# Performance work log

Hardware: AMD Instinct MI355X
Metric: run time of the kernel (lower is better)

The kernel has to match this reference:

```python
import jax, jax.numpy as jnp
import numpy as np

KAPPA = 0.1          # temperature for sinkhorn routing
SINK_ITERS = 3
SINK_EPS = 1e-6
NORM_EPS = 1e-12     # F.normalize clamp
LOG_EPS = 2.220446049250313e-16  # np.finfo(float).eps
K_TOP = 1


def _l2norm(v, axis=-1):
    n = jnp.sqrt(jnp.sum(v * v, axis=axis, keepdims=True))
    return v / jnp.maximum(n, NORM_EPS)


def _sinkhorn(log_alpha):
    # log_alpha: [K, N]
    L = jnp.exp(log_alpha)
    for _ in range(SINK_ITERS):
        L = L / (jnp.sum(L, axis=1, keepdims=True) + SINK_EPS)
        L = L / (jnp.sum(L, axis=0, keepdims=True) + SINK_EPS)
    return L


def setup_inputs() -> dict:
    key = jax.random.key(0)
    ks = jax.random.split(key, 16)
    dim = 1024
    N = 32768
    lora_dim = [8, 16, 32, 48, 64, 96, 128]
    inp = {
        "x": jax.random.normal(ks[0], (N, dim), dtype=jnp.float32),
        "prototypes": jax.random.normal(ks[1], (7, dim), dtype=jnp.float32),
    }
    for e, d in enumerate(lora_dim):
        # torch Linear weight: [out_features, in_features]
        inp[f"A{e}"] = jax.random.normal(ks[2 + 2 * e], (d, dim), dtype=jnp.float32) * (1.0 / np.sqrt(dim))
        inp[f"B{e}"] = jax.random.normal(ks[3 + 2 * e], (dim, d), dtype=jnp.float32) * (1.0 / np.sqrt(d))
    return inp


def reference(x, prototypes, A0, B0, A1, B1, A2, B2, A3, B3, A4, B4, A5, B5, A6, B6):
    A = [A0, A1, A2, A3, A4, A5, A6]
    B = [B0, B1, B2, B3, B4, B5, B6]
    N = x.shape[0]
    num_experts = len(A)

    # --- sinkhorn routing: gates [N, K] ---
    x_n = _l2norm(x)                       # [N, D]
    p_n = _l2norm(prototypes)              # [K, D]
    sim = jnp.einsum('kd,nd->kn', p_n, x_n)  # [K, N]
    L = _sinkhorn(sim / KAPPA)             # [K, N] doubly-stochastic-ish
    gates_full = L.T                       # [N, K]

    # --- top-k sparsification (k=1) ---
    top_vals, top_idx = jax.lax.top_k(gates_full, K_TOP)  # [N, k]
    gates = jnp.zeros_like(gates_full).at[jnp.arange(N)[:, None], top_idx].set(top_vals)

    # --- per-expert LoRA + weighted log-space combine ---
    # combine: out[b] = log( sum_e gates[b,e] * exp(B_e(A_e(x_b))) ), eps floor
    combined = jnp.zeros_like(x)
    for e in range(num_experts):
        y = jnp.einsum('nr,dr->nd', jnp.einsum('nd,rd->nr', x, A[e]), B[e])  # [N, D]
        combined = combined + gates[:, e:e + 1] * jnp.exp(y)
    combined = jnp.where(combined == 0, LOG_EPS, combined)
    return jnp.log(combined)
```

## Files before the change

### kernel.cpp

```cpp
#include <hip/hip_runtime.h>
#include <math.h>

#define NTOK 32768
#define DIM  1024
#define NE   7

#define PN_OFF   0
#define R1_OFF   7168
#define R2_OFF   7176
#define R3_OFF   7184
#define CNT_OFF  7192
#define PR1_OFF  7200
#define PR2_OFF  23584
#define PR3_OFF  24608
#define E0_OFF   25632
#define LG_OFF   287776
#define LIST_OFF 320544
#define A16_OFF  549920
#define B16_OFF  754720

#define SEPS 1e-6f

typedef __attribute__((ext_vector_type(8))) short short8v;
typedef __attribute__((ext_vector_type(4))) float f32x4;

constexpr int DV[7]   = {8, 16, 32, 48, 64, 96, 128};
constexpr int DPV[7]  = {32, 32, 32, 64, 64, 96, 128};
constexpr int DAPV[7] = {16, 16, 32, 48, 64, 96, 128};
constexpr int AOV[7]  = {0, 16384, 32768, 65536, 114688, 180224, 278528};
constexpr int BOV[7]  = {0, 32768, 65536, 98304, 163840, 229376, 327680};

struct ExpPtrs { const float* A[NE]; const float* B[NE]; };

__device__ __forceinline__ short f2bf(float f) {
  union { float f; unsigned u; } v; v.f = f;
  return (short)((v.u + 0x7FFFu + ((v.u >> 16) & 1u)) >> 16);
}

__device__ __forceinline__ float wsum(float v) {
  #pragma unroll
  for (int off = 32; off > 0; off >>= 1) v += __shfl_xor(v, off);
  return v;
}

__device__ __forceinline__ float dot4acc(float4 a, float4 b, float acc) {
  acc = fmaf(a.x, b.x, acc);
  acc = fmaf(a.y, b.y, acc);
  acc = fmaf(a.z, b.z, acc);
  acc = fmaf(a.w, b.w, acc);
  return acc;
}

__device__ __forceinline__ void ecfg(int e, int& d, int& dp, int& dap, int& ao, int& bo) {
  switch (e) {
    case 0: d = 8;   dp = 32;  dap = 16;  ao = 0;      bo = 0;      break;
    case 1: d = 16;  dp = 32;  dap = 16;  ao = 16384;  bo = 32768;  break;
    case 2: d = 32;  dp = 32;  dap = 32;  ao = 32768;  bo = 65536;  break;
    case 3: d = 48;  dp = 64;  dap = 48;  ao = 65536;  bo = 98304;  break;
    case 4: d = 64;  dp = 64;  dap = 64;  ao = 114688; bo = 163840; break;
    case 5: d = 96;  dp = 96;  dap = 96;  ao = 180224; bo = 229376; break;
    default: d = 128; dp = 128; dap = 128; ao = 278528; bo = 327680; break;
  }
}

__global__ __launch_bounds__(256) void k_conv(ExpPtrs p, short* __restrict__ A16,
                                              short* __restrict__ B16,
                                              const float* __restrict__ proto,
                                              float* __restrict__ wsf,
                                              int* __restrict__ counts) {
  const int e = blockIdx.y;
  const int tid = threadIdx.x;
  int d, dp, dap, ao, bo;
  ecfg(e, d, dp, dap, ao, bo);

  if (blockIdx.x == 0) {
    __shared__ float pred[4];
    if (e == 0 && tid < 8) counts[tid] = 0;
    const int w = tid >> 6, lane = tid & 63;
    float v4[4], ss = 0.f;
    #pragma unroll
    for (int i = 0; i < 4; ++i) {
      v4[i] = proto[e * DIM + tid + 256 * i];
      ss = fmaf(v4[i], v4[i], ss);
    }
    ss = wsum(ss);
    if (lane == 0) pred[w] = ss;
    __syncthreads();
    float tot = ((pred[0] + pred[1]) + pred[2]) + pred[3];
    float inv = 1.f / fmaxf(sqrtf(tot), 1e-12f);
    #pragma unroll
    for (int i = 0; i < 4; ++i)
      wsf[PN_OFF + e * DIM + tid + 256 * i] = v4[i] * inv;
  }

  const float* A = p.A[e];
  const float* B = p.B[e];
  short* Ad = A16 + ao;
  short* Bd = B16 + bo;
  const int t0 = blockIdx.x * 256 + tid;
  for (int i = t0; i < dap * DIM; i += 16 * 256) {
    int row = i >> 10;
    Ad[i] = (row < d) ? f2bf(A[i]) : (short)0;
  }
  for (int i = t0; i < DIM * dp; i += 16 * 256) {
    int j = i / dp, r = i - j * dp;
    Bd[i] = (r < d) ? f2bf(B[j * d + r]) : (short)0;
  }
}

__global__ __launch_bounds__(256) void k_sim(const float* __restrict__ x,
                                             const float* __restrict__ wsf,
                                             float* __restrict__ e0,
                                             float* __restrict__ pr1) {
  const int tid = threadIdx.x, w = tid >> 6, lane = tid & 63;
  const float4* pn4 = (const float4*)(wsf + PN_OFF);
  const int gw = blockIdx.x * 4 + w;
  float r1a[NE] = {0.f, 0.f, 0.f, 0.f, 0.f, 0.f, 0.f};
  for (int it = 0; it < 4; ++it) {
    const int n = gw + 8192 * it;
    const float4* xr4 = (const float4*)(x + (size_t)n * DIM);
    float xx = 0.f;
    float dk[NE] = {0.f, 0.f, 0.f, 0.f, 0.f, 0.f, 0.f};
    #pragma unroll
    for (int i = 0; i < 4; ++i) {
      float4 xv = xr4[lane + 64 * i];
      xx = dot4acc(xv, xv, xx);
      #pragma unroll
      for (int k = 0; k < NE; ++k)
        dk[k] = dot4acc(xv, pn4[k * 256 + lane + 64 * i], dk[k]);
    }
    xx = wsum(xx);
    #pragma unroll
    for (int k = 0; k < NE; ++k) dk[k] = wsum(dk[k]);
    if (lane == 0) {
      float nrm = fmaxf(sqrtf(xx), 1e-12f);
      #pragma unroll
      for (int k = 0; k < NE; ++k) {
        float ev = expf((dk[k] / nrm) / 0.1f);
        e0[(size_t)n * 8 + k] = ev;
        r1a[k] += ev;
      }
    }
  }
  __shared__ float red[4][8];
  if (lane == 0) {
    #pragma unroll
    for (int k = 0; k < NE; ++k) red[w][k] = r1a[k];
  }
  __syncthreads();
  if (tid == 0) {
    #pragma unroll
    for (int k = 0; k < NE; ++k)
      pr1[blockIdx.x * 8 + k] = ((red[0][k] + red[1][k]) + red[2][k]) + red[3][k];
  }
}

#define SUM7(l) (((((((l)[0] + (l)[1]) + (l)[2]) + (l)[3]) + (l)[4]) + (l)[5]) + (l)[6])

template<int DEPTH>
__global__ __launch_bounds__(256) void k_pass(const float* __restrict__ e0,
                                              float* __restrict__ wsf,
                                              const float* __restrict__ src, int nb,
                                              float* __restrict__ prOut,
                                              int* __restrict__ counts,
                                              int* __restrict__ list,
                                              float* __restrict__ lgv) {
  __shared__ float red2[8][33];
  __shared__ float Rcur[8];
  const int tid = threadIdx.x;
  {
    const int k = tid & 7, m = tid >> 3;
    float a = 0.f;
    for (int b = m; b < nb; b += 32) a += src[b * 8 + k];
    red2[k][m] = a;
    __syncthreads();
    if (tid < 8) {
      float s = 0.f;
      for (int mm = 0; mm < 32; ++mm) s += red2[tid][mm];
      Rcur[tid] = s;
      if (blockIdx.x == 0) {
        int roff = (DEPTH == 1) ? R1_OFF : (DEPTH == 2) ? R2_OFF : R3_OFF;
        wsf[roff + tid] = s;
      }
    }
    __syncthreads();
  }

  const int n = blockIdx.x * 256 + tid;
  float4 v0 = *(const float4*)(e0 + (size_t)n * 8);
  float4 v1 = *(const float4*)(e0 + (size_t)n * 8 + 4);
  float l[NE] = {v0.x, v0.y, v0.z, v0.w, v1.x, v1.y, v1.z};
  {
    const float* R1 = (DEPTH == 1) ? Rcur : (wsf + R1_OFF);
    #pragma unroll
    for (int k = 0; k < NE; ++k) l[k] = l[k] / (R1[k] + SEPS);
    float C = SUM7(l);
    #pragma unroll
    for (int k = 0; k < NE; ++k) l[k] = l[k] / (C + SEPS);
  }
  if constexpr (DEPTH >= 2) {
    const float* R2 = (DEPTH == 2) ? Rcur : (wsf + R2_OFF);
    #pragma unroll
    for (int k = 0; k < NE; ++k) l[k] = l[k] / (R2[k] + SEPS);
    float C = SUM7(l);
    #pragma unroll
    for (int k = 0; k < NE; ++k) l[k] = l[k] / (C + SEPS);
  }
  if constexpr (DEPTH >= 3) {
    const float* R3 = Rcur;
    #pragma unroll
    for (int k = 0; k < NE; ++k) l[k] = l[k] / (R3[k] + SEPS);
    float C = SUM7(l);
    #pragma unroll
    for (int k = 0; k < NE; ++k) l[k] = l[k] / (C + SEPS);
  }
  if constexpr (DEPTH == 3) {
    float best = l[0]; int be = 0;
    #pragma unroll
    for (int k = 1; k < NE; ++k) {
      if (l[k] > best) { best = l[k]; be = k; }
    }
    __shared__ int lcnt[8];
    __shared__ int wbase[4][8];
    __shared__ int gbase[8];
    const int w = tid >> 6, lane = tid & 63;
    if (tid < 8) lcnt[tid] = 0;
    __syncthreads();
    int rank = 0;
    #pragma unroll
    for (int k = 0; k < NE; ++k) {
      unsigned long long m = __ballot(be == k);
      if (lane == 0) wbase[w][k] = m ? atomicAdd(&lcnt[k], (int)__popcll(m)) : 0;
      if (be == k) rank = (int)__popcll(m & ((1ull << lane) - 1ull));
    }
    __syncthreads();
    if (tid < 8) gbase[tid] = lcnt[tid] ? atomicAdd(&counts[tid], lcnt[tid]) : 0;
    __syncthreads();
    int pos = gbase[be] + wbase[w][be] + rank;
    list[be * NTOK + pos] = n;
    lgv[n] = logf(best);
  } else {
    __shared__ float red[NE][256];
    #pragma unroll
    for (int k = 0; k < NE; ++k) red[k][tid] = l[k];
    __syncthreads();
    for (int off = 128; off > 0; off >>= 1) {
      if (tid < off) {
        #pragma unroll
        for (int k = 0; k < NE; ++k) red[k][tid] += red[k][tid + off];
      }
      __syncthreads();
    }
    if (tid < NE) prOut[blockIdx.x * 8 + tid] = red[tid][0];
  }
}

template<int E>
__device__ void expert_mfma(const float* __restrict__ x,
                            const short* __restrict__ A16,
                            const short* __restrict__ B16,
                            const int* __restrict__ list_e,
                            const float* __restrict__ lg,
                            int cnt, float* __restrict__ out,
                            char* lds) {
  constexpr int DP = DPV[E], DAP = DAPV[E];
  constexpr int NT1 = DAP / 16;
  constexpr int KS2 = DP / 32;
  constexpr int PP  = DAP + 4;
  constexpr int SP  = DP + 8;
  float* P = (float*)lds;
  short* T = (short*)(lds + 2 * 16 * PP * 4);

  const short* Am = A16 + AOV[E];
  const short* Bp = B16 + BOV[E];
  const int tid = threadIdx.x;
  const int w = tid >> 6, lane = tid & 63;
  const int lo = lane & 15, hi = lane >> 4;
  const int m0 = blockIdx.x * 16;

  const int myTok = list_e[min(m0 + lo, cnt - 1)];
  const float* xp = x + (size_t)myTok * DIM + w * 256 + hi * 8;
  const short* ApL = Am + lo * DIM + w * 256 + hi * 8;

  f32x4 acc1[NT1];
  #pragma unroll
  for (int t = 0; t < NT1; ++t) acc1[t] = (f32x4){0.f, 0.f, 0.f, 0.f};

  float4 nx0 = *(const float4*)(xp);
  float4 nx1 = *(const float4*)(xp + 4);
  #pragma unroll
  for (int kc = 0; kc < 256; kc += 32) {
    float4 x0 = nx0, x1 = nx1;
    if (kc + 32 < 256) {
      nx0 = *(const float4*)(xp + kc + 32);
      nx1 = *(const float4*)(xp + kc + 36);
    }
    short8v af;
    af[0] = f2bf(x0.x); af[1] = f2bf(x0.y); af[2] = f2bf(x0.z); af[3] = f2bf(x0.w);
    af[4] = f2bf(x1.x); af[5] = f2bf(x1.y); af[6] = f2bf(x1.z); af[7] = f2bf(x1.w);
    #pragma unroll
    for (int t = 0; t < NT1; ++t) {
      short8v bf = *(const short8v*)(ApL + t * 16 * DIM + kc);
      acc1[t] = __builtin_amdgcn_mfma_f32_16x16x32_bf16(af, bf, acc1[t], 0, 0, 0);
    }
  }

  float* Pw = P + (w & 1) * 16 * PP;
  if (w < 2) {
    #pragma unroll
    for (int t = 0; t < NT1; ++t)
      #pragma unroll
      for (int j = 0; j < 4; ++j)
        Pw[(hi * 4 + j) * PP + t * 16 + lo] = acc1[t][j];
  }
  __syncthreads();
  if (w >= 2) {
    #pragma unroll
    for (int t = 0; t < NT1; ++t)
      #pragma unroll
      for (int j = 0; j < 4; ++j)
        Pw[(hi * 4 + j) * PP + t * 16 + lo] += acc1[t][j];
  }
  __syncthreads();
  for (int i = tid; i < 16 * DP; i += 256) {
    int r = i / DP, c = i - r * DP;
    float v = (c < DAP) ? (P[r * PP + c] + P[(16 + r) * PP + c]) : 0.f;
    T[r * SP + c] = f2bf(v);
  }
  __syncthreads();

  short8v tf[KS2];
  #pragma unroll
  for (int ks = 0; ks < KS2; ++ks)
    tf[ks] = *(const short8v*)(T + lo * SP + ks * 32 + hi * 8);

  float  lgvr[4];
  float* op[4];
  #pragma unroll
  for (int j = 0; j < 4; ++j) {
    int t = list_e[min(m0 + hi * 4 + j, cnt - 1)];
    lgvr[j] = lg[t];
    op[j] = out + (size_t)t * DIM + w * 256 + lo;
  }

  const short* BpL = Bp + (size_t)(w * 256 + lo) * DP + hi * 8;
  #pragma unroll 4
  for (int nt = 0; nt < 16; ++nt) {
    f32x4 acc = (f32x4){0.f, 0.f, 0.f, 0.f};
    #pragma unroll
    for (int ks = 0; ks < KS2; ++ks) {
      short8v bf = *(const short8v*)(BpL + (size_t)nt * 16 * DP + ks * 32);
      acc = __builtin_amdgcn_mfma_f32_16x16x32_bf16(tf[ks], bf, acc, 0, 0, 0);
    }
    #pragma unroll
    for (int j = 0; j < 4; ++j)
      op[j][nt * 16] = acc[j] + lgvr[j];
  }
}

__global__ __launch_bounds__(256) void k_expert(const float* __restrict__ x,
                                                const short* __restrict__ A16,
                                                const short* __restrict__ B16,
                                                const int* __restrict__ list,
                                                const float* __restrict__ lg,
                                                const int* __restrict__ counts,
                                                float* __restrict__ out) {
  __shared__ __align__(16) char lds[21248];
  const int e = blockIdx.y;
  const int cnt = counts[e];
  if ((int)blockIdx.x * 16 >= cnt) return;
  switch (e) {
    case 0: expert_mfma<0>(x, A16, B16, list + 0 * NTOK, lg, cnt, out, lds); break;
    case 1: expert_mfma<1>(x, A16, B16, list + 1 * NTOK, lg, cnt, out, lds); break;
    case 2: expert_mfma<2>(x, A16, B16, list + 2 * NTOK, lg, cnt, out, lds); break;
    case 3: expert_mfma<3>(x, A16, B16, list + 3 * NTOK, lg, cnt, out, lds); break;
    case 4: expert_mfma<4>(x, A16, B16, list + 4 * NTOK, lg, cnt, out, lds); break;
    case 5: expert_mfma<5>(x, A16, B16, list + 5 * NTOK, lg, cnt, out, lds); break;
    case 6: expert_mfma<6>(x, A16, B16, list + 6 * NTOK, lg, cnt, out, lds); break;
  }
}

extern "C" void kernel_launch(void* const* d_in, const int* in_sizes, int n_in,
                              void* d_out, int out_size, void* d_ws, size_t ws_size,
                              hipStream_t stream) {
  const float* x     = (const float*)d_in[0];
  const float* proto = (const float*)d_in[1];
  ExpPtrs p;
  for (int e = 0; e < NE; ++e) {
    p.A[e] = (const float*)d_in[2 + 2 * e];
    p.B[e] = (const float*)d_in[3 + 2 * e];
  }
  float* wsf = (float*)d_ws;
  int*   wsi = (int*)d_ws;
  short* A16 = (short*)(wsf + A16_OFF);
  short* B16 = (short*)(wsf + B16_OFF);
  float* out = (float*)d_out;

  k_conv<<<dim3(16, NE), 256, 0, stream>>>(p, A16, B16, proto, wsf, wsi + CNT_OFF);
  k_sim<<<2048, 256, 0, stream>>>(x, wsf, wsf + E0_OFF, wsf + PR1_OFF);
  k_pass<1><<<128, 256, 0, stream>>>(wsf + E0_OFF, wsf, wsf + PR1_OFF, 2048,
                                     wsf + PR2_OFF, nullptr, nullptr, nullptr);
  k_pass<2><<<128, 256, 0, stream>>>(wsf + E0_OFF, wsf, wsf + PR2_OFF, 128,
                                     wsf + PR3_OFF, nullptr, nullptr, nullptr);
  k_pass<3><<<128, 256, 0, stream>>>(wsf + E0_OFF, wsf, wsf + PR3_OFF, 128,
                                     nullptr, wsi + CNT_OFF, wsi + LIST_OFF, wsf + LG_OFF);
  k_expert<<<dim3(2048, NE), 256, 0, stream>>>(x, A16, B16, wsi + LIST_OFF,
                                               wsf + LG_OFF, wsi + CNT_OFF, out);
}
```

Baseline: 195.0 us.

## Flatten expert grid into compact tile list and alias LDS staging buffers

Replaces the 2048x7 expert grid, where most blocks exit early, with a 1D grid of 2055 blocks. Each block walks the per-expert counts to find its expert and tile, so almost no launched blocks are idle. The bf16 staging buffer T now aliases the fp32 partial-sum buffer P: values are read into registers, a barrier is taken, then written back. This shrinks LDS per block so more blocks can be resident, at the cost of an extra barrier and a short serial scan over counts in every block.

```diff
diff --git a/kernel.cpp b/kernel.cpp
--- a/kernel.cpp
+++ b/kernel.cpp
@@ -261,7 +261,7 @@
                             const short* __restrict__ B16,
                             const int* __restrict__ list_e,
                             const float* __restrict__ lg,
-                            int cnt, float* __restrict__ out,
+                            int cnt, int tile, float* __restrict__ out,
                             char* lds) {
   constexpr int DP = DPV[E], DAP = DAPV[E];
   constexpr int NT1 = DAP / 16;
@@ -269,14 +269,14 @@
   constexpr int PP  = DAP + 4;
   constexpr int SP  = DP + 8;
   float* P = (float*)lds;
-  short* T = (short*)(lds + 2 * 16 * PP * 4);
+  short* T = (short*)lds;
 
   const short* Am = A16 + AOV[E];
   const short* Bp = B16 + BOV[E];
   const int tid = threadIdx.x;
   const int w = tid >> 6, lane = tid & 63;
   const int lo = lane & 15, hi = lane >> 4;
-  const int m0 = blockIdx.x * 16;
+  const int m0 = tile * 16;
 
   const int myTok = list_e[min(m0 + lo, cnt - 1)];
   const float* xp = x + (size_t)myTok * DIM + w * 256 + hi * 8;
@@ -322,10 +322,26 @@
         Pw[(hi * 4 + j) * PP + t * 16 + lo] += acc1[t][j];
   }
   __syncthreads();
-  for (int i = tid; i < 16 * DP; i += 256) {
-    int r = i / DP, c = i - r * DP;
-    float v = (c < DAP) ? (P[r * PP + c] + P[(16 + r) * PP + c]) : 0.f;
-    T[r * SP + c] = f2bf(v);
+  constexpr int NITEM = (16 * DP + 255) / 256;
+  float vloc[NITEM];
+  #pragma unroll
+  for (int it = 0; it < NITEM; ++it) {
+    int i = tid + it * 256;
+    float v = 0.f;
+    if (i < 16 * DP) {
+      int r = i / DP, c = i - r * DP;
+      if (c < DAP) v = P[r * PP + c] + P[(16 + r) * PP + c];
+    }
+    vloc[it] = v;
+  }
+  __syncthreads();
+  #pragma unroll
+  for (int it = 0; it < NITEM; ++it) {
+    int i = tid + it * 256;
+    if (i < 16 * DP) {
+      int r = i / DP, c = i - r * DP;
+      T[r * SP + c] = f2bf(vloc[it]);
+    }
   }
   __syncthreads();
 
@@ -365,18 +381,24 @@
                                                 const float* __restrict__ lg,
                                                 const int* __restrict__ counts,
                                                 float* __restrict__ out) {
-  __shared__ __align__(16) char lds[21248];
-  const int e = blockIdx.y;
-  const int cnt = counts[e];
-  if ((int)blockIdx.x * 16 >= cnt) return;
+  __shared__ __align__(16) char lds[16896];
+  int rem = blockIdx.x;
+  int e = 0, cnt;
+  while (true) {
+    cnt = counts[e];
+    int tiles = (cnt + 15) >> 4;
+    if (rem < tiles) break;
+    rem -= tiles;
+    if (++e == NE) return;
+  }
   switch (e) {
-    case 0: expert_mfma<0>(x, A16, B16, list + 0 * NTOK, lg, cnt, out, lds); break;
-    case 1: expert_mfma<1>(x, A16, B16, list + 1 * NTOK, lg, cnt, out, lds); break;
-    case 2: expert_mfma<2>(x, A16, B16, list + 2 * NTOK, lg, cnt, out, lds); break;
-    case 3: expert_mfma<3>(x, A16, B16, list + 3 * NTOK, lg, cnt, out, lds); break;
-    case 4: expert_mfma<4>(x, A16, B16, list + 4 * NTOK, lg, cnt, out, lds); break;
-    case 5: expert_mfma<5>(x, A16, B16, list + 5 * NTOK, lg, cnt, out, lds); break;
-    case 6: expert_mfma<6>(x, A16, B16, list + 6 * NTOK, lg, cnt, out, lds); break;
+    case 0: expert_mfma<0>(x, A16, B16, list + 0 * NTOK, lg, cnt, rem, out, lds); break;
+    case 1: expert_mfma<1>(x, A16, B16, list + 1 * NTOK, lg, cnt, rem, out, lds); break;
+    case 2: expert_mfma<2>(x, A16, B16, list + 2 * NTOK, lg, cnt, rem, out, lds); break;
+    case 3: expert_mfma<3>(x, A16, B16, list + 3 * NTOK, lg, cnt, rem, out, lds); break;
+    case 4: expert_mfma<4>(x, A16, B16, list + 4 * NTOK, lg, cnt, rem, out, lds); break;
+    case 5: expert_mfma<5>(x, A16, B16, list + 5 * NTOK, lg, cnt, rem, out, lds); break;
+    case 6: expert_mfma<6>(x, A16, B16, list + 6 * NTOK, lg, cnt, rem, out, lds); break;
   }
 }
 
@@ -404,6 +426,6 @@
                                      wsf + PR3_OFF, nullptr, nullptr, nullptr);
   k_pass<3><<<128, 256, 0, stream>>>(wsf + E0_OFF, wsf, wsf + PR3_OFF, 128,
                                      nullptr, wsi + CNT_OFF, wsi + LIST_OFF, wsf + LG_OFF);
-  k_expert<<<dim3(2048, NE), 256, 0, stream>>>(x, A16, B16, wsi + LIST_OFF,
-                                               wsf + LG_OFF, wsi + CNT_OFF, out);
-}
+  k_expert<<<2055, 256, 0, stream>>>(x, A16, B16, wsi + LIST_OFF,
+                                     wsf + LG_OFF, wsi + CNT_OFF, out);
+}
```

Result: no change. 192.9 us (-1.1%).

## Fuse all-expert A projection into similarity pass and compact expert launch

Applied to the files above, without the earlier changes.

The similarity kernel now streams each x tile once and, besides the prototype dot products, computes the A projections for all seven experts with MFMA, writing a bf16 low-rank buffer per token. The expert kernel then reads only this small buffer instead of re-reading x rows through the routing list, which removes the per-expert A GEMM and the LDS reduction. A flat 1D grid walks the expert counts so only populated tiles are launched. The cost is computing A projections for all experts on every token (about seven times the A work) plus an extra workspace write and read.

```diff
diff --git a/kernel.cpp b/kernel.cpp
--- a/kernel.cpp
+++ b/kernel.cpp
@@ -4,6 +4,7 @@
 #define NTOK 32768
 #define DIM  1024
 #define NE   7
+#define TROW 448
 
 #define PN_OFF   0
 #define R1_OFF   7168
@@ -18,6 +19,8 @@
 #define LIST_OFF 320544
 #define A16_OFF  549920
 #define B16_OFF  754720
+#define TALL_OFF_BYTES 3936384
+#define NBLK 2055
 
 #define SEPS 1e-6f
 
@@ -29,6 +32,10 @@
 constexpr int DAPV[7] = {16, 16, 32, 48, 64, 96, 128};
 constexpr int AOV[7]  = {0, 16384, 32768, 65536, 114688, 180224, 278528};
 constexpr int BOV[7]  = {0, 32768, 65536, 98304, 163840, 229376, 327680};
+constexpr int APRE[7] = {0, 32, 64, 96, 160, 224, 320};
+constexpr int TCOL[25] = {0, 32, 64, 80, 96, 112, 128, 160, 176, 192, 208,
+                          224, 240, 256, 272, 288, 304,
+                          320, 336, 352, 368, 384, 400, 416, 432};
 
 struct ExpPtrs { const float* A[NE]; const float* B[NE]; };
 
@@ -108,50 +115,106 @@
   }
 }
 
-__global__ __launch_bounds__(256) void k_sim(const float* __restrict__ x,
-                                             const float* __restrict__ wsf,
-                                             float* __restrict__ e0,
-                                             float* __restrict__ pr1) {
-  const int tid = threadIdx.x, w = tid >> 6, lane = tid & 63;
-  const float4* pn4 = (const float4*)(wsf + PN_OFF);
-  const int gw = blockIdx.x * 4 + w;
-  float r1a[NE] = {0.f, 0.f, 0.f, 0.f, 0.f, 0.f, 0.f};
-  for (int it = 0; it < 4; ++it) {
-    const int n = gw + 8192 * it;
-    const float4* xr4 = (const float4*)(x + (size_t)n * DIM);
-    float xx = 0.f;
-    float dk[NE] = {0.f, 0.f, 0.f, 0.f, 0.f, 0.f, 0.f};
-    #pragma unroll
-    for (int i = 0; i < 4; ++i) {
-      float4 xv = xr4[lane + 64 * i];
-      xx = dot4acc(xv, xv, xx);
+__global__ __launch_bounds__(512, 4) void k_simT(const float* __restrict__ x,
+                                                 const short* __restrict__ A16,
+                                                 const float* __restrict__ wsf,
+                                                 float* __restrict__ e0,
+                                                 float* __restrict__ pr1,
+                                                 short* __restrict__ Tall) {
+  __shared__ __align__(16) short As[400 * 40];
+  __shared__ float pnS[7][32];
+  __shared__ float prS[4][16][8];
+  const int tid = threadIdx.x;
+  const int n0 = blockIdx.x * 64;
+
+  for (int i = tid; i < 64 * 48; i += 512) {
+    int r = i / 48, c = i - r * 48;
+    int col = (c < 16) ? (16 + c) : ((c < 32) ? (32 + c) : (112 + c));
+    Tall[(size_t)(n0 + r) * TROW + col] = 0;
+  }
+
+  const int w = tid >> 6, lane = tid & 63, lo = lane & 15, hi = lane >> 4;
+  const int mh = w >> 1, nh = w & 1;
+  const int tokBase = n0 + mh * 16;
+  const int ts = nh * 12;
+  const float* xp = x + (size_t)(tokBase + lo) * DIM + hi * 8;
+  const float* PN = wsf + PN_OFF;
+
+  f32x4 acc[13];
+  #pragma unroll
+  for (int t = 0; t < 13; ++t) acc[t] = (f32x4){0.f, 0.f, 0.f, 0.f};
+  float dk[7] = {0.f, 0.f, 0.f, 0.f, 0.f, 0.f, 0.f};
+  float xx = 0.f;
+
+  for (int kc = 0; kc < DIM; kc += 32) {
+    for (int i = tid; i < 1600; i += 512) {
+      int r = i >> 2, q = i & 3;
+      *(short8v*)&As[r * 40 + q * 8] =
+          *(const short8v*)(A16 + (size_t)r * DIM + kc + q * 8);
+    }
+    if (tid < 224) pnS[tid >> 5][tid & 31] = PN[(tid >> 5) * DIM + kc + (tid & 31)];
+    __syncthreads();
+
+    float4 x0 = *(const float4*)(xp + kc);
+    float4 x1 = *(const float4*)(xp + kc + 4);
+    short8v af;
+    af[0] = f2bf(x0.x); af[1] = f2bf(x0.y); af[2] = f2bf(x0.z); af[3] = f2bf(x0.w);
+    af[4] = f2bf(x1.x); af[5] = f2bf(x1.y); af[6] = f2bf(x1.z); af[7] = f2bf(x1.w);
+
+    if (nh == 0) {
+      xx = dot4acc(x0, x0, dot4acc(x1, x1, xx));
       #pragma unroll
-      for (int k = 0; k < NE; ++k)
-        dk[k] = dot4acc(xv, pn4[k * 256 + lane + 64 * i], dk[k]);
-    }
-    xx = wsum(xx);
-    #pragma unroll
-    for (int k = 0; k < NE; ++k) dk[k] = wsum(dk[k]);
-    if (lane == 0) {
+      for (int k = 0; k < 7; ++k) {
+        float4 p0 = *(const float4*)&pnS[k][hi * 8];
+        float4 p1 = *(const float4*)&pnS[k][hi * 8 + 4];
+        dk[k] = dot4acc(x0, p0, dot4acc(x1, p1, dk[k]));
+      }
+    }
+    #pragma unroll
+    for (int tt = 0; tt < 13; ++tt) {
+      short8v bf = *(const short8v*)&As[(16 * (ts + tt) + lo) * 40 + hi * 8];
+      acc[tt] = __builtin_amdgcn_mfma_f32_16x16x32_bf16(af, bf, acc[tt], 0, 0, 0);
+    }
+    __syncthreads();
+  }
+
+  const int tw = 12 + nh;
+  #pragma unroll
+  for (int tt = 0; tt < 13; ++tt) {
+    if (tt < tw) {
+      int col = TCOL[ts + tt] + lo;
+      #pragma unroll
+      for (int j = 0; j < 4; ++j)
+        Tall[(size_t)(tokBase + hi * 4 + j) * TROW + col] = f2bf(acc[tt][j]);
+    }
+  }
+
+  if (nh == 0) {
+    #pragma unroll
+    for (int k = 0; k < 7; ++k) {
+      dk[k] += __shfl_xor(dk[k], 16);
+      dk[k] += __shfl_xor(dk[k], 32);
+    }
+    xx += __shfl_xor(xx, 16);
+    xx += __shfl_xor(xx, 32);
+    if (hi == 0) {
       float nrm = fmaxf(sqrtf(xx), 1e-12f);
+      int n = tokBase + lo;
       #pragma unroll
-      for (int k = 0; k < NE; ++k) {
+      for (int k = 0; k < 7; ++k) {
         float ev = expf((dk[k] / nrm) / 0.1f);
         e0[(size_t)n * 8 + k] = ev;
-        r1a[k] += ev;
+        prS[mh][lo][k] = ev;
       }
-    }
-  }
-  __shared__ float red[4][8];
-  if (lane == 0) {
-    #pragma unroll
-    for (int k = 0; k < NE; ++k) red[w][k] = r1a[k];
+      prS[mh][lo][7] = 0.f;
+    }
   }
   __syncthreads();
-  if (tid == 0) {
-    #pragma unroll
-    for (int k = 0; k < NE; ++k)
-      pr1[blockIdx.x * 8 + k] = ((red[0][k] + red[1][k]) + red[2][k]) + red[3][k];
+  if (tid < 8) {
+    float s = 0.f;
+    for (int m2 = 0; m2 < 4; ++m2)
+      for (int l2 = 0; l2 < 16; ++l2) s += prS[m2][l2][tid];
+    pr1[blockIdx.x * 8 + tid] = s;
   }
 }
 
@@ -255,96 +318,46 @@
   }
 }
 
+__device__ __forceinline__ bool walk(int bid, const int* counts,
+                                     int& e, int& tile, int& cnt) {
+  int rem = bid; e = 0;
+  while (true) {
+    cnt = counts[e];
+    int tiles = (cnt + 15) >> 4;
+    if (rem < tiles) { tile = rem; return true; }
+    rem -= tiles;
+    if (++e == NE) return false;
+  }
+}
+
 template<int E>
-__device__ void expert_mfma(const float* __restrict__ x,
-                            const short* __restrict__ A16,
-                            const short* __restrict__ B16,
-                            const int* __restrict__ list_e,
-                            const float* __restrict__ lg,
-                            int cnt, float* __restrict__ out,
-                            char* lds) {
-  constexpr int DP = DPV[E], DAP = DAPV[E];
-  constexpr int NT1 = DAP / 16;
+__device__ void phB_impl(const short* __restrict__ Bp,
+                         const short* __restrict__ Tall,
+                         const int* __restrict__ list_e,
+                         const float* __restrict__ lg,
+                         int cnt, int tile, float* __restrict__ out) {
+  constexpr int DP = DPV[E];
   constexpr int KS2 = DP / 32;
-  constexpr int PP  = DAP + 4;
-  constexpr int SP  = DP + 8;
-  float* P = (float*)lds;
-  short* T = (short*)(lds + 2 * 16 * PP * 4);
-
-  const short* Am = A16 + AOV[E];
-  const short* Bp = B16 + BOV[E];
   const int tid = threadIdx.x;
   const int w = tid >> 6, lane = tid & 63;
   const int lo = lane & 15, hi = lane >> 4;
-  const int m0 = blockIdx.x * 16;
+  const int m0 = tile * 16;
 
   const int myTok = list_e[min(m0 + lo, cnt - 1)];
-  const float* xp = x + (size_t)myTok * DIM + w * 256 + hi * 8;
-  const short* ApL = Am + lo * DIM + w * 256 + hi * 8;
-
-  f32x4 acc1[NT1];
-  #pragma unroll
-  for (int t = 0; t < NT1; ++t) acc1[t] = (f32x4){0.f, 0.f, 0.f, 0.f};
-
-  float4 nx0 = *(const float4*)(xp);
-  float4 nx1 = *(const float4*)(xp + 4);
-  #pragma unroll
-  for (int kc = 0; kc < 256; kc += 32) {
-    float4 x0 = nx0, x1 = nx1;
-    if (kc + 32 < 256) {
-      nx0 = *(const float4*)(xp + kc + 32);
-      nx1 = *(const float4*)(xp + kc + 36);
-    }
-    short8v af;
-    af[0] = f2bf(x0.x); af[1] = f2bf(x0.y); af[2] = f2bf(x0.z); af[3] = f2bf(x0.w);
-    af[4] = f2bf(x1.x); af[5] = f2bf(x1.y); af[6] = f2bf(x1.z); af[7] = f2bf(x1.w);
-    #pragma unroll
-    for (int t = 0; t < NT1; ++t) {
-      short8v bf = *(const short8v*)(ApL + t * 16 * DIM + kc);
-      acc1[t] = __builtin_amdgcn_mfma_f32_16x16x32_bf16(af, bf, acc1[t], 0, 0, 0);
-    }
-  }
-
-  float* Pw = P + (w & 1) * 16 * PP;
-  if (w < 2) {
-    #pragma unroll
-    for (int t = 0; t < NT1; ++t)
-      #pragma unroll
-      for (int j = 0; j < 4; ++j)
-        Pw[(hi * 4 + j) * PP + t * 16 + lo] = acc1[t][j];
-  }
-  __syncthreads();
-  if (w >= 2) {
-    #pragma unroll
-    for (int t = 0; t < NT1; ++t)
-      #pragma unroll
-      for (int j = 0; j < 4; ++j)
-        Pw[(hi * 4 + j) * PP + t * 16 + lo] += acc1[t][j];
-  }
-  __syncthreads();
-  for (int i = tid; i < 16 * DP; i += 256) {
-    int r = i / DP, c = i - r * DP;
-    float v = (c < DAP) ? (P[r * PP + c] + P[(16 + r) * PP + c]) : 0.f;
-    T[r * SP + c] = f2bf(v);
-  }
-  __syncthreads();
-
   short8v tf[KS2];
   #pragma unroll
   for (int ks = 0; ks < KS2; ++ks)
-    tf[ks] = *(const short8v*)(T + lo * SP + ks * 32 + hi * 8);
-
-  float  lgvr[4];
-  float* op[4];
+    tf[ks] = *(const short8v*)(Tall + (size_t)myTok * TROW + APRE[E] + ks * 32 + hi * 8);
+
+  int tok[4]; float lgvr[4];
   #pragma unroll
   for (int j = 0; j < 4; ++j) {
-    int t = list_e[min(m0 + hi * 4 + j, cnt - 1)];
-    lgvr[j] = lg[t];
-    op[j] = out + (size_t)t * DIM + w * 256 + lo;
+    tok[j] = list_e[min(m0 + hi * 4 + j, cnt - 1)];
+    lgvr[j] = lg[tok[j]];
   }
 
   const short* BpL = Bp + (size_t)(w * 256 + lo) * DP + hi * 8;
-  #pragma unroll 4
+  #pragma unroll 1
   for (int nt = 0; nt < 16; ++nt) {
     f32x4 acc = (f32x4){0.f, 0.f, 0.f, 0.f};
     #pragma unroll
@@ -354,29 +367,27 @@
     }
     #pragma unroll
     for (int j = 0; j < 4; ++j)
-      op[j][nt * 16] = acc[j] + lgvr[j];
-  }
-}
-
-__global__ __launch_bounds__(256) void k_expert(const float* __restrict__ x,
-                                                const short* __restrict__ A16,
-                                                const short* __restrict__ B16,
+      out[(size_t)tok[j] * DIM + w * 256 + nt * 16 + lo] = acc[j] + lgvr[j];
+  }
+}
+
+__global__ __launch_bounds__(256, 8) void k_phB(const short* __restrict__ B16,
+                                                const short* __restrict__ Tall,
                                                 const int* __restrict__ list,
                                                 const float* __restrict__ lg,
                                                 const int* __restrict__ counts,
                                                 float* __restrict__ out) {
-  __shared__ __align__(16) char lds[21248];
-  const int e = blockIdx.y;
-  const int cnt = counts[e];
-  if ((int)blockIdx.x * 16 >= cnt) return;
+  int bid = ((int)blockIdx.x * 1024) % NBLK;
+  int e, tile, cnt;
+  if (!walk(bid, counts, e, tile, cnt)) return;
   switch (e) {
-    case 0: expert_mfma<0>(x, A16, B16, list + 0 * NTOK, lg, cnt, out, lds); break;
-    case 1: expert_mfma<1>(x, A16, B16, list + 1 * NTOK, lg, cnt, out, lds); break;
-    case 2: expert_mfma<2>(x, A16, B16, list + 2 * NTOK, lg, cnt, out, lds); break;
-    case 3: expert_mfma<3>(x, A16, B16, list + 3 * NTOK, lg, cnt, out, lds); break;
-    case 4: expert_mfma<4>(x, A16, B16, list + 4 * NTOK, lg, cnt, out, lds); break;
-    case 5: expert_mfma<5>(x, A16, B16, list + 5 * NTOK, lg, cnt, out, lds); break;
-    case 6: expert_mfma<6>(x, A16, B16, list + 6 * NTOK, lg, cnt, out, lds); break;
+    case 0: phB_impl<0>(B16 + BOV[0], Tall, list + 0 * NTOK, lg, cnt, tile, out); break;
+    case 1: phB_impl<1>(B16 + BOV[1], Tall, list + 1 * NTOK, lg, cnt, tile, out); break;
+    case 2: phB_impl<2>(B16 + BOV[2], Tall, list + 2 * NTOK, lg, cnt, tile, out); break;
+    case 3: phB_impl<3>(B16 + BOV[3], Tall, list + 3 * NTOK, lg, cnt, tile, out); break;
+    case 4: phB_impl<4>(B16 + BOV[4], Tall, list + 4 * NTOK, lg, cnt, tile, out); break;
+    case 5: phB_impl<5>(B16 + BOV[5], Tall, list + 5 * NTOK, lg, cnt, tile, out); break;
+    default: phB_impl<6>(B16 + BOV[6], Tall, list + 6 * NTOK, lg, cnt, tile, out); break;
   }
 }
 
@@ -394,16 +405,17 @@
   int*   wsi = (int*)d_ws;
   short* A16 = (short*)(wsf + A16_OFF);
   short* B16 = (short*)(wsf + B16_OFF);
+  short* Tall = (short*)((char*)d_ws + TALL_OFF_BYTES);
   float* out = (float*)d_out;
 
   k_conv<<<dim3(16, NE), 256, 0, stream>>>(p, A16, B16, proto, wsf, wsi + CNT_OFF);
-  k_sim<<<2048, 256, 0, stream>>>(x, wsf, wsf + E0_OFF, wsf + PR1_OFF);
-  k_pass<1><<<128, 256, 0, stream>>>(wsf + E0_OFF, wsf, wsf + PR1_OFF, 2048,
+  k_simT<<<512, 512, 0, stream>>>(x, A16, wsf, wsf + E0_OFF, wsf + PR1_OFF, Tall);
+  k_pass<1><<<128, 256, 0, stream>>>(wsf + E0_OFF, wsf, wsf + PR1_OFF, 512,
                                      wsf + PR2_OFF, nullptr, nullptr, nullptr);
   k_pass<2><<<128, 256, 0, stream>>>(wsf + E0_OFF, wsf, wsf + PR2_OFF, 128,
                                      wsf + PR3_OFF, nullptr, nullptr, nullptr);
   k_pass<3><<<128, 256, 0, stream>>>(wsf + E0_OFF, wsf, wsf + PR3_OFF, 128,
                                      nullptr, wsi + CNT_OFF, wsi + LIST_OFF, wsf + LG_OFF);
-  k_expert<<<dim3(2048, NE), 256, 0, stream>>>(x, A16, B16, wsi + LIST_OFF,
-                                               wsf + LG_OFF, wsi + CNT_OFF, out);
-}
+  k_phB<<<NBLK, 256, 0, stream>>>(B16, Tall, wsi + LIST_OFF, wsf + LG_OFF,
+                                  wsi + CNT_OFF, out);
+}
```

After: 211.0 us. 1.08x slower.

## Re-layout A weights, drop cross-wave K-split reduction, compact expert tile grid

Applied to the files above, without the earlier changes.

Stores the bf16 A weights in a chunked image laid out by 32-column K-chunks, so each wave computes the full K=1024 projection for its 16-token tile on its own. This removes the LDS partial-sum reduction and the three block-wide barriers. The 2D grid of 2048x7 blocks, most of which exited early, becomes a compact 1D grid of 2055 tiles mapped onto experts by a prefix walk over counts, with a strided permutation of block ids. Each wave now redundantly reads all of x and A for the tile, so every block does four times the first-GEMM work in exchange for no synchronisation, and occupancy is set to 4 blocks via launch bounds.

```diff
diff --git a/kernel.cpp b/kernel.cpp
--- a/kernel.cpp
+++ b/kernel.cpp
@@ -16,8 +16,9 @@
 #define E0_OFF   25632
 #define LG_OFF   287776
 #define LIST_OFF 320544
-#define A16_OFF  549920
 #define B16_OFF  754720
+#define AIMG_OFF_BYTES 3936384
+#define NBLK 2055
 
 #define SEPS 1e-6f
 
@@ -27,14 +28,18 @@
 constexpr int DV[7]   = {8, 16, 32, 48, 64, 96, 128};
 constexpr int DPV[7]  = {32, 32, 32, 64, 64, 96, 128};
 constexpr int DAPV[7] = {16, 16, 32, 48, 64, 96, 128};
-constexpr int AOV[7]  = {0, 16384, 32768, 65536, 114688, 180224, 278528};
 constexpr int BOV[7]  = {0, 32768, 65536, 98304, 163840, 229376, 327680};
+constexpr int RSV[7]  = {0, 16, 32, 64, 112, 176, 272};
 
 struct ExpPtrs { const float* A[NE]; const float* B[NE]; };
 
 __device__ __forceinline__ short f2bf(float f) {
   union { float f; unsigned u; } v; v.f = f;
   return (short)((v.u + 0x7FFFu + ((v.u >> 16) & 1u)) >> 16);
+}
+
+__device__ __forceinline__ unsigned packbf(float a, float b) {
+  return (unsigned)(unsigned short)f2bf(a) | ((unsigned)(unsigned short)f2bf(b) << 16);
 }
 
 __device__ __forceinline__ float wsum(float v) {
@@ -51,27 +56,14 @@
   return acc;
 }
 
-__device__ __forceinline__ void ecfg(int e, int& d, int& dp, int& dap, int& ao, int& bo) {
-  switch (e) {
-    case 0: d = 8;   dp = 32;  dap = 16;  ao = 0;      bo = 0;      break;
-    case 1: d = 16;  dp = 32;  dap = 16;  ao = 16384;  bo = 32768;  break;
-    case 2: d = 32;  dp = 32;  dap = 32;  ao = 32768;  bo = 65536;  break;
-    case 3: d = 48;  dp = 64;  dap = 48;  ao = 65536;  bo = 98304;  break;
-    case 4: d = 64;  dp = 64;  dap = 64;  ao = 114688; bo = 163840; break;
-    case 5: d = 96;  dp = 96;  dap = 96;  ao = 180224; bo = 229376; break;
-    default: d = 128; dp = 128; dap = 128; ao = 278528; bo = 327680; break;
-  }
-}
-
-__global__ __launch_bounds__(256) void k_conv(ExpPtrs p, short* __restrict__ A16,
+__global__ __launch_bounds__(256) void k_conv(ExpPtrs p, short* __restrict__ AIMG,
                                               short* __restrict__ B16,
                                               const float* __restrict__ proto,
                                               float* __restrict__ wsf,
                                               int* __restrict__ counts) {
   const int e = blockIdx.y;
   const int tid = threadIdx.x;
-  int d, dp, dap, ao, bo;
-  ecfg(e, d, dp, dap, ao, bo);
+  const int d = DV[e], dp = DPV[e], dap = DAPV[e], bo = BOV[e], rs = RSV[e];
 
   if (blockIdx.x == 0) {
     __shared__ float pred[4];
@@ -95,16 +87,25 @@
 
   const float* A = p.A[e];
   const float* B = p.B[e];
-  short* Ad = A16 + ao;
+  const int t0 = blockIdx.x * 256 + tid;
+
+  const int tot = dap * 128;
+  for (int i = t0; i < tot; i += 16 * 256) {
+    int lr = i >> 7, rem = i & 127;
+    int c = rem >> 2, q = rem & 3;
+    short8v v = (short8v){0, 0, 0, 0, 0, 0, 0, 0};
+    if (lr < d) {
+      const float* src = A + (size_t)lr * DIM + c * 32 + q * 8;
+      #pragma unroll
+      for (int j = 0; j < 8; ++j) v[j] = f2bf(src[j]);
+    }
+    *(short8v*)&AIMG[c * 12800 + (rs + lr) * 32 + q * 8] = v;
+  }
+
   short* Bd = B16 + bo;
-  const int t0 = blockIdx.x * 256 + tid;
-  for (int i = t0; i < dap * DIM; i += 16 * 256) {
-    int row = i >> 10;
-    Ad[i] = (row < d) ? f2bf(A[i]) : (short)0;
-  }
   for (int i = t0; i < DIM * dp; i += 16 * 256) {
     int j = i / dp, r = i - j * dp;
-    Bd[i] = (r < d) ? f2bf(B[j * d + r]) : (short)0;
+    Bd[i] = (r < d) ? f2bf(B[(size_t)j * d + r]) : (short)0;
   }
 }
 
@@ -257,30 +258,27 @@
 
 template<int E>
 __device__ void expert_mfma(const float* __restrict__ x,
-                            const short* __restrict__ A16,
+                            const short* __restrict__ AIMG,
                             const short* __restrict__ B16,
                             const int* __restrict__ list_e,
                             const float* __restrict__ lg,
-                            int cnt, float* __restrict__ out,
-                            char* lds) {
+                            int cnt, int tile, float* __restrict__ out,
+                            short* Tlds) {
   constexpr int DP = DPV[E], DAP = DAPV[E];
   constexpr int NT1 = DAP / 16;
   constexpr int KS2 = DP / 32;
-  constexpr int PP  = DAP + 4;
   constexpr int SP  = DP + 8;
-  float* P = (float*)lds;
-  short* T = (short*)(lds + 2 * 16 * PP * 4);
-
-  const short* Am = A16 + AOV[E];
+  const int rs = RSV[E];
   const short* Bp = B16 + BOV[E];
   const int tid = threadIdx.x;
   const int w = tid >> 6, lane = tid & 63;
   const int lo = lane & 15, hi = lane >> 4;
-  const int m0 = blockIdx.x * 16;
+  const int m0 = tile * 16;
+  short* T = Tlds + w * 16 * 136;
 
   const int myTok = list_e[min(m0 + lo, cnt - 1)];
-  const float* xp = x + (size_t)myTok * DIM + w * 256 + hi * 8;
-  const short* ApL = Am + lo * DIM + w * 256 + hi * 8;
+  const float* xp = x + (size_t)myTok * DIM + hi * 8;
+  const short* Ab = AIMG + (rs + lo) * 32 + hi * 8;
 
   f32x4 acc1[NT1];
   #pragma unroll
@@ -288,63 +286,49 @@
 
   float4 nx0 = *(const float4*)(xp);
   float4 nx1 = *(const float4*)(xp + 4);
-  #pragma unroll
-  for (int kc = 0; kc < 256; kc += 32) {
+  for (int c = 0; c < 32; ++c) {
     float4 x0 = nx0, x1 = nx1;
-    if (kc + 32 < 256) {
-      nx0 = *(const float4*)(xp + kc + 32);
-      nx1 = *(const float4*)(xp + kc + 36);
+    if (c < 31) {
+      nx0 = *(const float4*)(xp + (c + 1) * 32);
+      nx1 = *(const float4*)(xp + (c + 1) * 32 + 4);
     }
     short8v af;
     af[0] = f2bf(x0.x); af[1] = f2bf(x0.y); af[2] = f2bf(x0.z); af[3] = f2bf(x0.w);
     af[4] = f2bf(x1.x); af[5] = f2bf(x1.y); af[6] = f2bf(x1.z); af[7] = f2bf(x1.w);
+    const short* Ac = Ab + c * 12800;
     #pragma unroll
     for (int t = 0; t < NT1; ++t) {
-      short8v bf = *(const short8v*)(ApL + t * 16 * DIM + kc);
-      acc1[t] = __builtin_amdgcn_mfma_f32_16x16x32_bf16(af, bf, acc1[t], 0, 0, 0);
-    }
-  }
-
-  float* Pw = P + (w & 1) * 16 * PP;
-  if (w < 2) {
-    #pragma unroll
-    for (int t = 0; t < NT1; ++t)
-      #pragma unroll
-      for (int j = 0; j < 4; ++j)
-        Pw[(hi * 4 + j) * PP + t * 16 + lo] = acc1[t][j];
-  }
-  __syncthreads();
-  if (w >= 2) {
-    #pragma unroll
-    for (int t = 0; t < NT1; ++t)
-      #pragma unroll
-      for (int j = 0; j < 4; ++j)
-        Pw[(hi * 4 + j) * PP + t * 16 + lo] += acc1[t][j];
-  }
-  __syncthreads();
-  for (int i = tid; i < 16 * DP; i += 256) {
-    int r = i / DP, c = i - r * DP;
-    float v = (c < DAP) ? (P[r * PP + c] + P[(16 + r) * PP + c]) : 0.f;
-    T[r * SP + c] = f2bf(v);
-  }
-  __syncthreads();
+      short8v Af = *(const short8v*)(Ac + t * 512);
+      acc1[t] = __builtin_amdgcn_mfma_f32_16x16x32_bf16(Af, af, acc1[t], 0, 0, 0);
+    }
+  }
+
+  #pragma unroll
+  for (int t = 0; t < NT1; ++t) {
+    uint2 uv;
+    uv.x = packbf(acc1[t][0], acc1[t][1]);
+    uv.y = packbf(acc1[t][2], acc1[t][3]);
+    *(uint2*)&T[lo * SP + t * 16 + hi * 4] = uv;
+  }
+  if constexpr (DAP < DP) {
+    uint2 z; z.x = 0; z.y = 0;
+    *(uint2*)&T[lo * SP + DAP + hi * 4] = z;
+  }
 
   short8v tf[KS2];
   #pragma unroll
   for (int ks = 0; ks < KS2; ++ks)
     tf[ks] = *(const short8v*)(T + lo * SP + ks * 32 + hi * 8);
 
-  float  lgvr[4];
-  float* op[4];
+  int tok[4]; float lgvr[4];
   #pragma unroll
   for (int j = 0; j < 4; ++j) {
-    int t = list_e[min(m0 + hi * 4 + j, cnt - 1)];
-    lgvr[j] = lg[t];
-    op[j] = out + (size_t)t * DIM + w * 256 + lo;
+    tok[j] = list_e[min(m0 + hi * 4 + j, cnt - 1)];
+    lgvr[j] = lg[tok[j]];
   }
 
   const short* BpL = Bp + (size_t)(w * 256 + lo) * DP + hi * 8;
-  #pragma unroll 4
+  #pragma unroll 1
   for (int nt = 0; nt < 16; ++nt) {
     f32x4 acc = (f32x4){0.f, 0.f, 0.f, 0.f};
     #pragma unroll
@@ -354,29 +338,36 @@
     }
     #pragma unroll
     for (int j = 0; j < 4; ++j)
-      op[j][nt * 16] = acc[j] + lgvr[j];
-  }
-}
-
-__global__ __launch_bounds__(256) void k_expert(const float* __restrict__ x,
-                                                const short* __restrict__ A16,
-                                                const short* __restrict__ B16,
-                                                const int* __restrict__ list,
-                                                const float* __restrict__ lg,
-                                                const int* __restrict__ counts,
-                                                float* __restrict__ out) {
-  __shared__ __align__(16) char lds[21248];
-  const int e = blockIdx.y;
-  const int cnt = counts[e];
-  if ((int)blockIdx.x * 16 >= cnt) return;
+      out[(size_t)tok[j] * DIM + w * 256 + nt * 16 + lo] = acc[j] + lgvr[j];
+  }
+}
+
+__global__ __launch_bounds__(256, 4) void k_expert(const float* __restrict__ x,
+                                                   const short* __restrict__ AIMG,
+                                                   const short* __restrict__ B16,
+                                                   const int* __restrict__ list,
+                                                   const float* __restrict__ lg,
+                                                   const int* __restrict__ counts,
+                                                   float* __restrict__ out) {
+  __shared__ __align__(16) short Tlds[4 * 16 * 136];
+  int bid = ((int)blockIdx.x * 1024) % NBLK;
+  int rem = bid;
+  int e = 0, cnt;
+  while (true) {
+    cnt = counts[e];
+    int tiles = (cnt + 15) >> 4;
+    if (rem < tiles) break;
+    rem -= tiles;
+    if (++e == NE) return;
+  }
   switch (e) {
-    case 0: expert_mfma<0>(x, A16, B16, list + 0 * NTOK, lg, cnt, out, lds); break;
-    case 1: expert_mfma<1>(x, A16, B16, list + 1 * NTOK, lg, cnt, out, lds); break;
-    case 2: expert_mfma<2>(x, A16, B16, list + 2 * NTOK, lg, cnt, out, lds); break;
-    case 3: expert_mfma<3>(x, A16, B16, list + 3 * NTOK, lg, cnt, out, lds); break;
-    case 4: expert_mfma<4>(x, A16, B16, list + 4 * NTOK, lg, cnt, out, lds); break;
-    case 5: expert_mfma<5>(x, A16, B16, list + 5 * NTOK, lg, cnt, out, lds); break;
-    case 6: expert_mfma<6>(x, A16, B16, list + 6 * NTOK, lg, cnt, out, lds); break;
+    case 0: expert_mfma<0>(x, AIMG, B16, list + 0 * NTOK, lg, cnt, rem, out, Tlds); break;
+    case 1: expert_mfma<1>(x, AIMG, B16, list + 1 * NTOK, lg, cnt, rem, out, Tlds); break;
+    case 2: expert_mfma<2>(x, AIMG, B16, list + 2 * NTOK, lg, cnt, rem, out, Tlds); break;
+    case 3: expert_mfma<3>(x, AIMG, B16, list + 3 * NTOK, lg, cnt, rem, out, Tlds); break;
+    case 4: expert_mfma<4>(x, AIMG, B16, list + 4 * NTOK, lg, cnt, rem, out, Tlds); break;
+    case 5: expert_mfma<5>(x, AIMG, B16, list + 5 * NTOK, lg, cnt, rem, out, Tlds); break;
+    case 6: expert_mfma<6>(x, AIMG, B16, list + 6 * NTOK, lg, cnt, rem, out, Tlds); break;
   }
 }
 
@@ -390,13 +381,13 @@
     p.A[e] = (const float*)d_in[2 + 2 * e];
     p.B[e] = (const float*)d_in[3 + 2 * e];
   }
-  float* wsf = (float*)d_ws;
-  int*   wsi = (int*)d_ws;
-  short* A16 = (short*)(wsf + A16_OFF);
-  short* B16 = (short*)(wsf + B16_OFF);
-  float* out = (float*)d_out;
-
-  k_conv<<<dim3(16, NE), 256, 0, stream>>>(p, A16, B16, proto, wsf, wsi + CNT_OFF);
+  float* wsf  = (float*)d_ws;
+  int*   wsi  = (int*)d_ws;
+  short* B16  = (short*)(wsf + B16_OFF);
+  short* AIMG = (short*)((char*)d_ws + AIMG_OFF_BYTES);
+  float* out  = (float*)d_out;
+
+  k_conv<<<dim3(16, NE), 256, 0, stream>>>(p, AIMG, B16, proto, wsf, wsi + CNT_OFF);
   k_sim<<<2048, 256, 0, stream>>>(x, wsf, wsf + E0_OFF, wsf + PR1_OFF);
   k_pass<1><<<128, 256, 0, stream>>>(wsf + E0_OFF, wsf, wsf + PR1_OFF, 2048,
                                      wsf + PR2_OFF, nullptr, nullptr, nullptr);
@@ -404,6 +395,6 @@
                                      wsf + PR3_OFF, nullptr, nullptr, nullptr);
   k_pass<3><<<128, 256, 0, stream>>>(wsf + E0_OFF, wsf, wsf + PR3_OFF, 128,
                                      nullptr, wsi + CNT_OFF, wsi + LIST_OFF, wsf + LG_OFF);
-  k_expert<<<dim3(2048, NE), 256, 0, stream>>>(x, A16, B16, wsi + LIST_OFF,
-                                               wsf + LG_OFF, wsi + CNT_OFF, out);
-}
+  k_expert<<<NBLK, 256, 0, stream>>>(x, AIMG, B16, wsi + LIST_OFF,
+                                     wsf + LG_OFF, wsi + CNT_OFF, out);
+}
```

Result: slower. 262.3 us (+34.5%).
